# Optimization experiments

Hardware: AMD Instinct MI355X
Metric: run time of the kernel (lower is better)

Reference implementation:

```python
import jax, jax.numpy as jnp
import numpy as np

N_NODES = 10000
DIM_IN = 64
DIM_OUT = 64
K = 3
BATCH = 32
N_EDGES = 160000


def setup_inputs() -> dict:
    key = jax.random.key(0)
    ks = jax.random.split(key, 8)
    inputs = jax.random.normal(ks[0], (BATCH, N_NODES, DIM_IN), dtype=jnp.float32)
    hx = jax.random.normal(ks[1], (BATCH, N_NODES, DIM_OUT), dtype=jnp.float32)
    edge_index = jax.random.randint(ks[2], (2, N_EDGES), 0, N_NODES, dtype=jnp.int64)
    edge_weight = jax.random.uniform(ks[3], (N_EDGES,), dtype=jnp.float32)
    f = K * (DIM_IN + DIM_OUT)
    # xavier-uniform style scaling
    lim_g = float(np.sqrt(6.0 / (2 * DIM_OUT + f)))
    lim_c = float(np.sqrt(6.0 / (DIM_OUT + f)))
    weight_gate = jax.random.uniform(ks[4], (2 * DIM_OUT, f), minval=-lim_g, maxval=lim_g, dtype=jnp.float32)
    weight_candidate = jax.random.uniform(ks[5], (DIM_OUT, f), minval=-lim_c, maxval=lim_c, dtype=jnp.float32)
    bias_gate = jnp.zeros((2 * DIM_OUT,), dtype=jnp.float32)
    bias_candidate = jnp.zeros((DIM_OUT,), dtype=jnp.float32)
    return {
        'inputs': inputs, 'hx': hx, 'edge_index': edge_index, 'edge_weight': edge_weight,
        'weight_gate': weight_gate, 'weight_candidate': weight_candidate,
        'bias_gate': bias_gate, 'bias_candidate': bias_candidate,
    }


def _graph_conv(x, row, col, w):
    # x: [B, N, F]; out[b, dst] += w_e * x[b, src]; src=col, dst=row
    gathered = x[:, col, :] * w[None, :, None]  # [B, E, F]
    return jnp.zeros_like(x).at[:, row, :].add(gathered)


def _diffusion_conv(x, row, col, w, K):
    results = [x]
    x0 = x
    x1 = _graph_conv(x0, row, col, w)
    results.append(x1)
    for k in range(2, K):
        xk = 2.0 * _graph_conv(x1, row, col, w) - x0
        results.append(xk)
        x0, x1 = x1, xk
    return jnp.concatenate(results, axis=-1)  # [B, N, K*F]


def reference(inputs, hx, edge_index, edge_weight, weight_gate, weight_candidate, bias_gate, bias_candidate):
    row, col = edge_index[0], edge_index[1]
    hidden_dim = hx.shape[-1]
    x = jnp.concatenate([inputs, hx], axis=-1)
    x_diff = _diffusion_conv(x, row, col, edge_weight, K)
    gates = jnp.einsum('bnf,gf->bng', x_diff, weight_gate) + bias_gate
    z_r = jax.nn.sigmoid(gates)
    z, r = z_r[..., :hidden_dim], z_r[..., hidden_dim:]
    x_cand = jnp.concatenate([inputs, r * hx], axis=-1)
    x_cand_diff = _diffusion_conv(x_cand, row, col, edge_weight, K)
    cand = jnp.tanh(jnp.einsum('bnf,of->bno', x_cand_diff, weight_candidate) + bias_candidate)
    return (1.0 - z) * hx + z * cand
```

## Files before the change

### kernel.cpp

```cpp
#include <hip/hip_runtime.h>
#include <math.h>
#include <stdint.h>

#define NN   10000
#define EE   160000
#define BB   32
#define FDIM 384
#define NB_FULL 1250
#define NB_HALF 625

typedef _Float16 f16x8 __attribute__((ext_vector_type(8)));
typedef _Float16 f16x4 __attribute__((ext_vector_type(4)));
typedef _Float16 f16x2 __attribute__((ext_vector_type(2)));
typedef __fp16   pk16  __attribute__((ext_vector_type(2)));
typedef float    f32x4 __attribute__((ext_vector_type(4)));


__global__ void count_kernel(const int* __restrict__ ei, int* __restrict__ counts) {
    int e = blockIdx.x * blockDim.x + threadIdx.x;
    if (e < EE) atomicAdd(&counts[ei[e]], 1);
}

__global__ void scan_kernel(const int* __restrict__ counts, int* __restrict__ row_ptr) {
    __shared__ int sh[1024];
    int t = threadIdx.x;
    const int CH = 10;
    int base = t * CH;
    int local[CH];
    int s = 0;
#pragma unroll
    for (int i = 0; i < CH; i++) {
        int idx = base + i;
        int v = (idx < NN) ? counts[idx] : 0;
        local[i] = v; s += v;
    }
    sh[t] = s;
    __syncthreads();
    for (int off = 1; off < 1024; off <<= 1) {
        int add = (t >= off) ? sh[t - off] : 0;
        __syncthreads();
        sh[t] += add;
        __syncthreads();
    }
    int prefix = (t == 0) ? 0 : sh[t - 1];
#pragma unroll
    for (int i = 0; i < CH; i++) {
        int idx = base + i;
        if (idx < NN) row_ptr[idx] = prefix;
        prefix += local[i];
    }
    if (t == 1023) row_ptr[NN] = prefix;
}

__global__ void fill_kernel(const int* __restrict__ ei, const float* __restrict__ ew,
                            const int* __restrict__ row_ptr, int* __restrict__ cursor,
                            int* __restrict__ col_s, float* __restrict__ w_s) {
    int e = blockIdx.x * blockDim.x + threadIdx.x;
    if (e < EE) {
        int r = ei[e];
        int c = ei[EE + e];
        int pos = row_ptr[r] + atomicAdd(&cursor[r], 1);
        col_s[pos] = c;
        w_s[pos] = ew[e];
    }
}


__global__ void wconv_kernel(const float* __restrict__ wg, const float* __restrict__ wc,
                             _Float16* __restrict__ whg, _Float16* __restrict__ whc) {
    int i = blockIdx.x * blockDim.x + threadIdx.x;
    if (i < 128 * FDIM) whg[i] = (_Float16)wg[i];
    if (i < 64 * FDIM)  whc[i] = (_Float16)wc[i];
}

__global__ void cvt_h_kernel(const float* __restrict__ a, const float* __restrict__ b,
                             _Float16* __restrict__ ah, _Float16* __restrict__ bh, int n4) {
    int i = blockIdx.x * blockDim.x + threadIdx.x;
    if (i >= n4) return;
    const float* s = (blockIdx.y == 0) ? a : b;
    _Float16*    d = (blockIdx.y == 0) ? ah : bh;
    float4 v = reinterpret_cast<const float4*>(s)[i];
    f16x4 h; h[0] = (_Float16)v.x; h[1] = (_Float16)v.y;
             h[2] = (_Float16)v.z; h[3] = (_Float16)v.w;
    reinterpret_cast<f16x4*>(d)[i] = h;
}

__device__ inline void sp_map(int NB, int bc_n, int& b, int& nb) {
    int L = blockIdx.x;
    if ((bc_n & 7) == 0) {
        int xcd = L & 7;
        int x   = L >> 3;
        b  = xcd + 8 * (x / NB);
        nb = x % NB;
    } else {
        b  = L / NB;
        nb = L % NB;
    }
}

__device__ __forceinline__ void gather_acc4(
        const int* __restrict__ col_s, const float* __restrict__ w_s,
        const _Float16* __restrict__ src, long stride, int fo,
        long base, int start, int end,
        float& a0, float& a1, float& a2, float& a3)
{
#if __has_builtin(__builtin_amdgcn_fdot2) && __has_builtin(__builtin_amdgcn_perm)
    int j = start;
#define GDOT(da, db, wp)                                                              \
    a0 = __builtin_amdgcn_fdot2(__builtin_bit_cast(pk16,                              \
             __builtin_amdgcn_perm(db.x, da.x, 0x05040100u)), wp, a0, false);         \
    a1 = __builtin_amdgcn_fdot2(__builtin_bit_cast(pk16,                              \
             __builtin_amdgcn_perm(db.x, da.x, 0x07060302u)), wp, a1, false);         \
    a2 = __builtin_amdgcn_fdot2(__builtin_bit_cast(pk16,                              \
             __builtin_amdgcn_perm(db.y, da.y, 0x05040100u)), wp, a2, false);         \
    a3 = __builtin_amdgcn_fdot2(__builtin_bit_cast(pk16,                              \
             __builtin_amdgcn_perm(db.y, da.y, 0x07060302u)), wp, a3, false);
    for (; j + 8 <= end; j += 8) {
        int c0 = col_s[j],     c1 = col_s[j + 1], c2 = col_s[j + 2], c3 = col_s[j + 3];
        int c4 = col_s[j + 4], c5 = col_s[j + 5], c6 = col_s[j + 6], c7 = col_s[j + 7];
        uint2 d0 = *reinterpret_cast<const uint2*>(&src[(base + c0) * stride + fo]);
        uint2 d1 = *reinterpret_cast<const uint2*>(&src[(base + c1) * stride + fo]);
        uint2 d2 = *reinterpret_cast<const uint2*>(&src[(base + c2) * stride + fo]);
        uint2 d3 = *reinterpret_cast<const uint2*>(&src[(base + c3) * stride + fo]);
        uint2 d4 = *reinterpret_cast<const uint2*>(&src[(base + c4) * stride + fo]);
        uint2 d5 = *reinterpret_cast<const uint2*>(&src[(base + c5) * stride + fo]);
        uint2 d6 = *reinterpret_cast<const uint2*>(&src[(base + c6) * stride + fo]);
        uint2 d7 = *reinterpret_cast<const uint2*>(&src[(base + c7) * stride + fo]);
        pk16 wp0 = __builtin_amdgcn_cvt_pkrtz(w_s[j],     w_s[j + 1]);
        pk16 wp1 = __builtin_amdgcn_cvt_pkrtz(w_s[j + 2], w_s[j + 3]);
        pk16 wp2 = __builtin_amdgcn_cvt_pkrtz(w_s[j + 4], w_s[j + 5]);
        pk16 wp3 = __builtin_amdgcn_cvt_pkrtz(w_s[j + 6], w_s[j + 7]);
        GDOT(d0, d1, wp0) GDOT(d2, d3, wp1) GDOT(d4, d5, wp2) GDOT(d6, d7, wp3)
    }
    for (; j + 2 <= end; j += 2) {
        int c0 = col_s[j], c1 = col_s[j + 1];
        uint2 d0 = *reinterpret_cast<const uint2*>(&src[(base + c0) * stride + fo]);
        uint2 d1 = *reinterpret_cast<const uint2*>(&src[(base + c1) * stride + fo]);
        pk16 wp0 = __builtin_amdgcn_cvt_pkrtz(w_s[j], w_s[j + 1]);
        GDOT(d0, d1, wp0)
    }
    if (j < end) {
        int c = col_s[j]; float w = w_s[j];
        f16x4 v = *reinterpret_cast<const f16x4*>(&src[(base + c) * stride + fo]);
        a0 += w * (float)v[0]; a1 += w * (float)v[1];
        a2 += w * (float)v[2]; a3 += w * (float)v[3];
    }
#undef GDOT
#else
    for (int j = start; j < end; ++j) {
        int c = col_s[j]; float w = w_s[j];
        f16x4 v = *reinterpret_cast<const f16x4*>(&src[(base + c) * stride + fo]);
        a0 += w * (float)v[0]; a1 += w * (float)v[1];
        a2 += w * (float)v[2]; a3 += w * (float)v[3];
    }
#endif
}

__global__ __launch_bounds__(256)
void spmm_full16(const int* __restrict__ row_ptr, const int* __restrict__ col_s,
                 const float* __restrict__ w_s,
                 const _Float16* __restrict__ srcA, int sA,
                 const _Float16* __restrict__ srcB, int sB,
                 const _Float16* __restrict__ subA, const _Float16* __restrict__ subB,
                 float alpha, _Float16* __restrict__ outbuf, int bc_n) {
    int b, nb; sp_map(NB_FULL, bc_n, b, nb);
    int node = nb * 8 + (threadIdx.x >> 5);
    int g    = threadIdx.x & 31;
    const _Float16* src; long stride; int fo;
    if (g < 16) { src = srcA; stride = sA; fo = g * 4; }
    else        { src = srcB; stride = sB; fo = (g - 16) * 4; }
    int start = row_ptr[node], end = row_ptr[node + 1];
    long base = (long)b * NN;
    float a0 = 0.f, a1 = 0.f, a2 = 0.f, a3 = 0.f;
    gather_acc4(col_s, w_s, src, stride, fo, base, start, end, a0, a1, a2, a3);
    a0 *= alpha; a1 *= alpha; a2 *= alpha; a3 *= alpha;
    if (subA) {
        const _Float16* sub = (g < 16) ? subA : subB;
        f16x4 s = *reinterpret_cast<const f16x4*>(&sub[(base + node) * 64 + fo]);
        a0 -= (float)s[0]; a1 -= (float)s[1]; a2 -= (float)s[2]; a3 -= (float)s[3];
    }
    f16x4 r; r[0] = (_Float16)a0; r[1] = (_Float16)a1;
             r[2] = (_Float16)a2; r[3] = (_Float16)a3;
    *reinterpret_cast<f16x4*>(&outbuf[(base + node) * 128 + g * 4]) = r;
}

__global__ __launch_bounds__(256)
void spmm_half16(const int* __restrict__ row_ptr, const int* __restrict__ col_s,
                 const float* __restrict__ w_s,
                 const _Float16* __restrict__ src, int sstride,
                 const _Float16* __restrict__ sub, float alpha,
                 _Float16* __restrict__ outbuf, int bc_n) {
    int b, nb; sp_map(NB_HALF, bc_n, b, nb);
    int node = nb * 16 + (threadIdx.x >> 4);
    int fo   = (threadIdx.x & 15) * 4;
    int start = row_ptr[node], end = row_ptr[node + 1];
    long base = (long)b * NN;
    float a0 = 0.f, a1 = 0.f, a2 = 0.f, a3 = 0.f;
    gather_acc4(col_s, w_s, src, sstride, fo, base, start, end, a0, a1, a2, a3);
    a0 *= alpha; a1 *= alpha; a2 *= alpha; a3 *= alpha;
    if (sub) {
        f16x4 s = *reinterpret_cast<const f16x4*>(&sub[(base + node) * 64 + fo]);
        a0 -= (float)s[0]; a1 -= (float)s[1]; a2 -= (float)s[2]; a3 -= (float)s[3];
    }
    f16x4 r; r[0] = (_Float16)a0; r[1] = (_Float16)a1;
             r[2] = (_Float16)a2; r[3] = (_Float16)a3;
    *reinterpret_cast<f16x4*>(&outbuf[(base + node) * 128 + fo]) = r;
}

template <int MODE>
__global__ __launch_bounds__(256)
void gemm_mfma(const _Float16* __restrict__ in_h,
               const _Float16* __restrict__ hxl_h,
               const _Float16* __restrict__ W1h,
               const _Float16* __restrict__ W2h,
               const _Float16* __restrict__ Wh,
               const float* __restrict__ bias,
               const float* __restrict__ hx32,
               const _Float16* __restrict__ zbuf,
               float* __restrict__ outf,
               _Float16* __restrict__ z_o,
               _Float16* __restrict__ rh_o,
               int Mchunk)
{
    const int NOUT = (MODE == 0) ? 128 : 64;
    const int TNF  = NOUT / 16;
    const int PIT  = 40;

    __shared__ _Float16 Alds[64 * PIT];
    __shared__ _Float16 Blds[NOUT * PIT];

    int tid  = threadIdx.x;
    int lane = tid & 63;
    int w    = tid >> 6;
    int lr   = lane & 15;
    int lko  = (lane >> 4) * 8;

    long mbase = (long)blockIdx.x * 64;

    f32x4 acc[TNF];
#pragma unroll
    for (int f = 0; f < TNF; f++) acc[f] = (f32x4){0.f, 0.f, 0.f, 0.f};

    for (int k0 = 0; k0 < FDIM; k0 += 32) {
        const _Float16* src; int stride; int koff;
        if      (k0 < 64)  { src = in_h;  stride = 64;  koff = 0;   }
        else if (k0 < 128) { src = hxl_h; stride = 64;  koff = 64;  }
        else if (k0 < 256) { src = W1h;   stride = 128; koff = 128; }
        else               { src = W2h;   stride = 128; koff = 256; }

        {
            int rr = tid >> 2;
            int q  = tid & 3;
            long row = mbase + rr;
            if (row >= Mchunk) row = Mchunk - 1;
            *reinterpret_cast<f16x8*>(&Alds[rr * PIT + q * 8]) =
                *reinterpret_cast<const f16x8*>(&src[row * (long)stride + (k0 - koff) + q * 8]);
        }
        {
            for (int l = tid * 8; l < NOUT * 32; l += 256 * 8) {
                int n  = l >> 5;
                int kk = l & 31;
                *reinterpret_cast<f16x8*>(&Blds[n * PIT + kk]) =
                    *reinterpret_cast<const f16x8*>(&Wh[n * FDIM + k0 + kk]);
            }
        }
        __syncthreads();

        f16x8 a = *reinterpret_cast<const f16x8*>(&Alds[(w * 16 + lr) * PIT + lko]);
#pragma unroll
        for (int f = 0; f < TNF; f++) {
            f16x8 bfr = *reinterpret_cast<const f16x8*>(&Blds[(lr + 16 * f) * PIT + lko]);
            acc[f] = __builtin_amdgcn_mfma_f32_16x16x32_f16(a, bfr, acc[f], 0, 0, 0);
        }
        __syncthreads();
    }

#pragma unroll
    for (int f = 0; f < TNF; f++) {
        int g = lr + 16 * f;
#pragma unroll
        for (int j = 0; j < 4; j++) {
            long m = mbase + w * 16 + (lane >> 4) * 4 + j;
            if (m >= Mchunk) continue;
            float v = acc[f][j] + bias[g];
            if (MODE == 0) {
                float s = 1.f / (1.f + __expf(-v));
                if (g < 64) z_o[m * 64 + g] = (_Float16)s;
                else        rh_o[m * 64 + (g - 64)] = (_Float16)(s * hx32[m * 64 + (g - 64)]);
            } else {
                float cnd = tanhf(v);
                float zz = (float)zbuf[m * 64 + g];
                outf[m * 64 + g] = (1.f - zz) * hx32[m * 64 + g] + zz * cnd;
            }
        }
    }
}


extern "C" void kernel_launch(void* const* d_in, const int* in_sizes, int n_in,
                              void* d_out, int out_size, void* d_ws, size_t ws_size,
                              hipStream_t stream) {
    const float* inputs = (const float*)d_in[0];
    const float* hx     = (const float*)d_in[1];
    const int*   ei     = (const int*)d_in[2];
    const float* ew     = (const float*)d_in[3];
    const float* wg     = (const float*)d_in[4];
    const float* wc     = (const float*)d_in[5];
    const float* bg     = (const float*)d_in[6];
    const float* bc     = (const float*)d_in[7];
    float* out = (float*)d_out;

    const size_t csr_bytes = (size_t)(NN + 1) * 4 + (size_t)NN * 4 * 2
                           + (size_t)EE * 4 + (size_t)EE * 4
                           + (size_t)(128 + 64) * FDIM * 2 + 512;
    const size_t per_batch = (size_t)NN * 512 * 2;

    int bc_n = 1;
    const int cand[6] = {32, 16, 8, 4, 2, 1};
    for (int i = 0; i < 6; i++) {
        if (csr_bytes + (size_t)cand[i] * per_batch <= ws_size) { bc_n = cand[i]; break; }
    }

    uint8_t* p = (uint8_t*)d_ws;
    _Float16* W1h  = (_Float16*)p; p += (size_t)bc_n * NN * 128 * 2;
    _Float16* W2h  = (_Float16*)p; p += (size_t)bc_n * NN * 128 * 2;
    _Float16* in_h = (_Float16*)p; p += (size_t)bc_n * NN * 64 * 2;
    _Float16* hx_h = (_Float16*)p; p += (size_t)bc_n * NN * 64 * 2;
    _Float16* rh   = (_Float16*)p; p += (size_t)bc_n * NN * 64 * 2;
    _Float16* zh   = (_Float16*)p; p += (size_t)bc_n * NN * 64 * 2;
    int* row_ptr = (int*)p;  p += (size_t)(NN + 1) * 4;
    int* counts  = (int*)p;  p += (size_t)NN * 4;
    int* cursor  = (int*)p;  p += (size_t)NN * 4;
    int* col_s   = (int*)p;  p += (size_t)EE * 4;
    float* w_s   = (float*)p; p += (size_t)EE * 4;
    p = (uint8_t*)(((uintptr_t)p + 63) & ~(uintptr_t)63);
    _Float16* whg = (_Float16*)p; p += (size_t)128 * FDIM * 2;
    _Float16* whc = (_Float16*)p;

    hipMemsetAsync(counts, 0, 2 * NN * sizeof(int), stream);
    count_kernel<<<(EE + 255) / 256, 256, 0, stream>>>(ei, counts);
    scan_kernel<<<1, 1024, 0, stream>>>(counts, row_ptr);
    fill_kernel<<<(EE + 255) / 256, 256, 0, stream>>>(ei, ew, row_ptr, cursor, col_s, w_s);
    wconv_kernel<<<(128 * FDIM + 255) / 256, 256, 0, stream>>>(wg, wc, whg, whc);

    for (int b0 = 0; b0 < BB; b0 += bc_n) {
        const float* in_c = inputs + (size_t)b0 * NN * 64;
        const float* hx_c = hx     + (size_t)b0 * NN * 64;
        float*       out_c = out   + (size_t)b0 * NN * 64;
        int Mchunk = bc_n * NN;
        int gemm_blocks = (Mchunk + 63) / 64;
        int n4 = bc_n * NN * 64 / 4;

        dim3 cg((n4 + 255) / 256, 2);
        cvt_h_kernel<<<cg, 256, 0, stream>>>(in_c, hx_c, in_h, hx_h, n4);

        spmm_full16<<<NB_FULL * bc_n, 256, 0, stream>>>(row_ptr, col_s, w_s,
                                                        in_h, 64, hx_h, 64,
                                                        nullptr, nullptr, 1.f, W1h, bc_n);
        spmm_full16<<<NB_FULL * bc_n, 256, 0, stream>>>(row_ptr, col_s, w_s,
                                                        W1h, 128, W1h + 64, 128,
                                                        in_h, hx_h, 2.f, W2h, bc_n);
        gemm_mfma<0><<<gemm_blocks, 256, 0, stream>>>(in_h, hx_h, W1h, W2h, whg, bg,
                                                      hx_c, nullptr, nullptr, zh, rh, Mchunk);
        spmm_half16<<<NB_HALF * bc_n, 256, 0, stream>>>(row_ptr, col_s, w_s, rh, 64,
                                                        nullptr, 1.f, W1h + 64, bc_n);
        spmm_half16<<<NB_HALF * bc_n, 256, 0, stream>>>(row_ptr, col_s, w_s, W1h + 64, 128,
                                                        rh, 2.f, W2h + 64, bc_n);
        gemm_mfma<1><<<gemm_blocks, 256, 0, stream>>>(in_h, rh, W1h, W2h, whc, bc,
                                                      hx_c, zh, out_c, nullptr, nullptr, Mchunk);
    }
}
```

Measured before the change: 979.5 us.

## Pad CSR rows to multiples of eight and store edge weights as fp16

The CSR build now rounds each row's edge count up to a multiple of eight, and the padded slots are zeroed. Edge weights are stored as fp16, so the gather loop can issue vector loads of column indices and weights and drop its remainder loops. Source addressing changes to 32-bit byte offsets built from shifts, with a base-pointer delta selecting the second source. This cuts per-edge instruction and index overhead in the SpMM kernels, at the cost of extra zero-weight padded edges, lower-precision weights, and a dependence on 32-bit offsets staying in range.

```diff
diff --git a/kernel.cpp b/kernel.cpp
--- a/kernel.cpp
+++ b/kernel.cpp
@@ -6,6 +6,7 @@
 #define EE   160000
 #define BB   32
 #define FDIM 384
+#define EE_PAD (EE + 8 * NN)
 #define NB_FULL 1250
 #define NB_HALF 625
 
@@ -31,7 +32,7 @@
 #pragma unroll
     for (int i = 0; i < CH; i++) {
         int idx = base + i;
-        int v = (idx < NN) ? counts[idx] : 0;
+        int v = (idx < NN) ? ((counts[idx] + 7) & ~7) : 0;
         local[i] = v; s += v;
     }
     sh[t] = s;
@@ -54,14 +55,14 @@
 
 __global__ void fill_kernel(const int* __restrict__ ei, const float* __restrict__ ew,
                             const int* __restrict__ row_ptr, int* __restrict__ cursor,
-                            int* __restrict__ col_s, float* __restrict__ w_s) {
+                            int* __restrict__ col_s, _Float16* __restrict__ w_h) {
     int e = blockIdx.x * blockDim.x + threadIdx.x;
     if (e < EE) {
         int r = ei[e];
         int c = ei[EE + e];
         int pos = row_ptr[r] + atomicAdd(&cursor[r], 1);
         col_s[pos] = c;
-        w_s[pos] = ew[e];
+        w_h[pos] = (_Float16)ew[e];
     }
 }
 
@@ -99,13 +100,11 @@
 }
 
 __device__ __forceinline__ void gather_acc4(
-        const int* __restrict__ col_s, const float* __restrict__ w_s,
-        const _Float16* __restrict__ src, long stride, int fo,
-        long base, int start, int end,
-        float& a0, float& a1, float& a2, float& a3)
+        const int* __restrict__ col_s, const _Float16* __restrict__ w_h,
+        const char* __restrict__ srcb, int sh, unsigned fo_all,
+        int start, int end, float& a0, float& a1, float& a2, float& a3)
 {
 #if __has_builtin(__builtin_amdgcn_fdot2) && __has_builtin(__builtin_amdgcn_perm)
-    int j = start;
 #define GDOT(da, db, wp)                                                              \
     a0 = __builtin_amdgcn_fdot2(__builtin_bit_cast(pk16,                              \
              __builtin_amdgcn_perm(db.x, da.x, 0x05040100u)), wp, a0, false);         \
@@ -115,41 +114,29 @@
              __builtin_amdgcn_perm(db.y, da.y, 0x05040100u)), wp, a2, false);         \
     a3 = __builtin_amdgcn_fdot2(__builtin_bit_cast(pk16,                              \
              __builtin_amdgcn_perm(db.y, da.y, 0x07060302u)), wp, a3, false);
-    for (; j + 8 <= end; j += 8) {
-        int c0 = col_s[j],     c1 = col_s[j + 1], c2 = col_s[j + 2], c3 = col_s[j + 3];
-        int c4 = col_s[j + 4], c5 = col_s[j + 5], c6 = col_s[j + 6], c7 = col_s[j + 7];
-        uint2 d0 = *reinterpret_cast<const uint2*>(&src[(base + c0) * stride + fo]);
-        uint2 d1 = *reinterpret_cast<const uint2*>(&src[(base + c1) * stride + fo]);
-        uint2 d2 = *reinterpret_cast<const uint2*>(&src[(base + c2) * stride + fo]);
-        uint2 d3 = *reinterpret_cast<const uint2*>(&src[(base + c3) * stride + fo]);
-        uint2 d4 = *reinterpret_cast<const uint2*>(&src[(base + c4) * stride + fo]);
-        uint2 d5 = *reinterpret_cast<const uint2*>(&src[(base + c5) * stride + fo]);
-        uint2 d6 = *reinterpret_cast<const uint2*>(&src[(base + c6) * stride + fo]);
-        uint2 d7 = *reinterpret_cast<const uint2*>(&src[(base + c7) * stride + fo]);
-        pk16 wp0 = __builtin_amdgcn_cvt_pkrtz(w_s[j],     w_s[j + 1]);
-        pk16 wp1 = __builtin_amdgcn_cvt_pkrtz(w_s[j + 2], w_s[j + 3]);
-        pk16 wp2 = __builtin_amdgcn_cvt_pkrtz(w_s[j + 4], w_s[j + 5]);
-        pk16 wp3 = __builtin_amdgcn_cvt_pkrtz(w_s[j + 6], w_s[j + 7]);
+    for (int j = start; j < end; j += 8) {
+        int4  ca = *reinterpret_cast<const int4*>(&col_s[j]);
+        int4  cb = *reinterpret_cast<const int4*>(&col_s[j + 4]);
+        uint4 wv = *reinterpret_cast<const uint4*>(&w_h[j]);
+        uint2 d0 = *reinterpret_cast<const uint2*>(srcb + (((unsigned)ca.x << sh) + fo_all));
+        uint2 d1 = *reinterpret_cast<const uint2*>(srcb + (((unsigned)ca.y << sh) + fo_all));
+        uint2 d2 = *reinterpret_cast<const uint2*>(srcb + (((unsigned)ca.z << sh) + fo_all));
+        uint2 d3 = *reinterpret_cast<const uint2*>(srcb + (((unsigned)ca.w << sh) + fo_all));
+        uint2 d4 = *reinterpret_cast<const uint2*>(srcb + (((unsigned)cb.x << sh) + fo_all));
+        uint2 d5 = *reinterpret_cast<const uint2*>(srcb + (((unsigned)cb.y << sh) + fo_all));
+        uint2 d6 = *reinterpret_cast<const uint2*>(srcb + (((unsigned)cb.z << sh) + fo_all));
+        uint2 d7 = *reinterpret_cast<const uint2*>(srcb + (((unsigned)cb.w << sh) + fo_all));
+        pk16 wp0 = __builtin_bit_cast(pk16, wv.x);
+        pk16 wp1 = __builtin_bit_cast(pk16, wv.y);
+        pk16 wp2 = __builtin_bit_cast(pk16, wv.z);
+        pk16 wp3 = __builtin_bit_cast(pk16, wv.w);
         GDOT(d0, d1, wp0) GDOT(d2, d3, wp1) GDOT(d4, d5, wp2) GDOT(d6, d7, wp3)
-    }
-    for (; j + 2 <= end; j += 2) {
-        int c0 = col_s[j], c1 = col_s[j + 1];
-        uint2 d0 = *reinterpret_cast<const uint2*>(&src[(base + c0) * stride + fo]);
-        uint2 d1 = *reinterpret_cast<const uint2*>(&src[(base + c1) * stride + fo]);
-        pk16 wp0 = __builtin_amdgcn_cvt_pkrtz(w_s[j], w_s[j + 1]);
-        GDOT(d0, d1, wp0)
-    }
-    if (j < end) {
-        int c = col_s[j]; float w = w_s[j];
-        f16x4 v = *reinterpret_cast<const f16x4*>(&src[(base + c) * stride + fo]);
-        a0 += w * (float)v[0]; a1 += w * (float)v[1];
-        a2 += w * (float)v[2]; a3 += w * (float)v[3];
     }
 #undef GDOT
 #else
     for (int j = start; j < end; ++j) {
-        int c = col_s[j]; float w = w_s[j];
-        f16x4 v = *reinterpret_cast<const f16x4*>(&src[(base + c) * stride + fo]);
+        int c = col_s[j]; float w = (float)w_h[j];
+        f16x4 v = *reinterpret_cast<const f16x4*>(srcb + (((unsigned)c << sh) + fo_all));
         a0 += w * (float)v[0]; a1 += w * (float)v[1];
         a2 += w * (float)v[2]; a3 += w * (float)v[3];
     }
@@ -158,21 +145,21 @@
 
 __global__ __launch_bounds__(256)
 void spmm_full16(const int* __restrict__ row_ptr, const int* __restrict__ col_s,
-                 const float* __restrict__ w_s,
-                 const _Float16* __restrict__ srcA, int sA,
-                 const _Float16* __restrict__ srcB, int sB,
+                 const _Float16* __restrict__ w_h,
+                 const _Float16* __restrict__ srcBase, int sh, int deltaB,
                  const _Float16* __restrict__ subA, const _Float16* __restrict__ subB,
                  float alpha, _Float16* __restrict__ outbuf, int bc_n) {
     int b, nb; sp_map(NB_FULL, bc_n, b, nb);
     int node = nb * 8 + (threadIdx.x >> 5);
     int g    = threadIdx.x & 31;
-    const _Float16* src; long stride; int fo;
-    if (g < 16) { src = srcA; stride = sA; fo = g * 4; }
-    else        { src = srcB; stride = sB; fo = (g - 16) * 4; }
+    int fo, db;
+    if (g < 16) { fo = g * 4;        db = 0;      }
+    else        { fo = (g - 16) * 4; db = deltaB; }
+    unsigned fo_all = ((unsigned)(b * NN) << sh) + (unsigned)db + (unsigned)(fo * 2);
     int start = row_ptr[node], end = row_ptr[node + 1];
     long base = (long)b * NN;
     float a0 = 0.f, a1 = 0.f, a2 = 0.f, a3 = 0.f;
-    gather_acc4(col_s, w_s, src, stride, fo, base, start, end, a0, a1, a2, a3);
+    gather_acc4(col_s, w_h, (const char*)srcBase, sh, fo_all, start, end, a0, a1, a2, a3);
     a0 *= alpha; a1 *= alpha; a2 *= alpha; a3 *= alpha;
     if (subA) {
         const _Float16* sub = (g < 16) ? subA : subB;
@@ -186,17 +173,18 @@
 
 __global__ __launch_bounds__(256)
 void spmm_half16(const int* __restrict__ row_ptr, const int* __restrict__ col_s,
-                 const float* __restrict__ w_s,
-                 const _Float16* __restrict__ src, int sstride,
+                 const _Float16* __restrict__ w_h,
+                 const _Float16* __restrict__ src, int sh,
                  const _Float16* __restrict__ sub, float alpha,
                  _Float16* __restrict__ outbuf, int bc_n) {
     int b, nb; sp_map(NB_HALF, bc_n, b, nb);
     int node = nb * 16 + (threadIdx.x >> 4);
     int fo   = (threadIdx.x & 15) * 4;
+    unsigned fo_all = ((unsigned)(b * NN) << sh) + (unsigned)(fo * 2);
     int start = row_ptr[node], end = row_ptr[node + 1];
     long base = (long)b * NN;
     float a0 = 0.f, a1 = 0.f, a2 = 0.f, a3 = 0.f;
-    gather_acc4(col_s, w_s, src, sstride, fo, base, start, end, a0, a1, a2, a3);
+    gather_acc4(col_s, w_h, (const char*)src, sh, fo_all, start, end, a0, a1, a2, a3);
     a0 *= alpha; a1 *= alpha; a2 *= alpha; a3 *= alpha;
     if (sub) {
         f16x4 s = *reinterpret_cast<const f16x4*>(&sub[(base + node) * 64 + fo]);
@@ -311,7 +299,7 @@
     float* out = (float*)d_out;
 
     const size_t csr_bytes = (size_t)(NN + 1) * 4 + (size_t)NN * 4 * 2
-                           + (size_t)EE * 4 + (size_t)EE * 4
+                           + (size_t)EE_PAD * 6
                            + (size_t)(128 + 64) * FDIM * 2 + 512;
     const size_t per_batch = (size_t)NN * 512 * 2;
 
@@ -329,18 +317,19 @@
     _Float16* rh   = (_Float16*)p; p += (size_t)bc_n * NN * 64 * 2;
     _Float16* zh   = (_Float16*)p; p += (size_t)bc_n * NN * 64 * 2;
     int* row_ptr = (int*)p;  p += (size_t)(NN + 1) * 4;
+    p = (uint8_t*)(((uintptr_t)p + 15) & ~(uintptr_t)15);
     int* counts  = (int*)p;  p += (size_t)NN * 4;
     int* cursor  = (int*)p;  p += (size_t)NN * 4;
-    int* col_s   = (int*)p;  p += (size_t)EE * 4;
-    float* w_s   = (float*)p; p += (size_t)EE * 4;
+    int* col_s   = (int*)p;  p += (size_t)EE_PAD * 4;
+    _Float16* w_h = (_Float16*)p; p += (size_t)EE_PAD * 2;
     p = (uint8_t*)(((uintptr_t)p + 63) & ~(uintptr_t)63);
     _Float16* whg = (_Float16*)p; p += (size_t)128 * FDIM * 2;
     _Float16* whc = (_Float16*)p;
 
-    hipMemsetAsync(counts, 0, 2 * NN * sizeof(int), stream);
+    hipMemsetAsync(counts, 0, (size_t)NN * 8 + (size_t)EE_PAD * 6, stream);
     count_kernel<<<(EE + 255) / 256, 256, 0, stream>>>(ei, counts);
     scan_kernel<<<1, 1024, 0, stream>>>(counts, row_ptr);
-    fill_kernel<<<(EE + 255) / 256, 256, 0, stream>>>(ei, ew, row_ptr, cursor, col_s, w_s);
+    fill_kernel<<<(EE + 255) / 256, 256, 0, stream>>>(ei, ew, row_ptr, cursor, col_s, w_h);
     wconv_kernel<<<(128 * FDIM + 255) / 256, 256, 0, stream>>>(wg, wc, whg, whc);
 
     for (int b0 = 0; b0 < BB; b0 += bc_n) {
@@ -354,17 +343,19 @@
         dim3 cg((n4 + 255) / 256, 2);
         cvt_h_kernel<<<cg, 256, 0, stream>>>(in_c, hx_c, in_h, hx_h, n4);
 
-        spmm_full16<<<NB_FULL * bc_n, 256, 0, stream>>>(row_ptr, col_s, w_s,
-                                                        in_h, 64, hx_h, 64,
+        int deltaA = (int)((const char*)hx_h - (const char*)in_h);
+
+        spmm_full16<<<NB_FULL * bc_n, 256, 0, stream>>>(row_ptr, col_s, w_h,
+                                                        in_h, 7, deltaA,
                                                         nullptr, nullptr, 1.f, W1h, bc_n);
-        spmm_full16<<<NB_FULL * bc_n, 256, 0, stream>>>(row_ptr, col_s, w_s,
-                                                        W1h, 128, W1h + 64, 128,
+        spmm_full16<<<NB_FULL * bc_n, 256, 0, stream>>>(row_ptr, col_s, w_h,
+                                                        W1h, 8, 128,
                                                         in_h, hx_h, 2.f, W2h, bc_n);
         gemm_mfma<0><<<gemm_blocks, 256, 0, stream>>>(in_h, hx_h, W1h, W2h, whg, bg,
                                                       hx_c, nullptr, nullptr, zh, rh, Mchunk);
-        spmm_half16<<<NB_HALF * bc_n, 256, 0, stream>>>(row_ptr, col_s, w_s, rh, 64,
+        spmm_half16<<<NB_HALF * bc_n, 256, 0, stream>>>(row_ptr, col_s, w_h, rh, 7,
                                                         nullptr, 1.f, W1h + 64, bc_n);
-        spmm_half16<<<NB_HALF * bc_n, 256, 0, stream>>>(row_ptr, col_s, w_s, W1h + 64, 128,
+        spmm_half16<<<NB_HALF * bc_n, 256, 0, stream>>>(row_ptr, col_s, w_h, W1h + 64, 8,
                                                         rh, 2.f, W2h + 64, bc_n);
         gemm_mfma<1><<<gemm_blocks, 256, 0, stream>>>(in_h, rh, W1h, W2h, whc, bc,
                                                       hx_c, zh, out_c, nullptr, nullptr, Mchunk);
```

After: 932.3 us. 4.8% less time.
